# Kernel tuning notes

Hardware: AMD Instinct MI355X
Metric: run time of the kernel (lower is better)

The kernel has to match this reference:

```python
import jax, jax.numpy as jnp
import numpy as np

D = 1024   # hidden_size
H = 16     # n_head
K = 64     # head_size
B = 4
T = 1024
LAYER_ID = 12
NUM_LAYERS = 24
D_MIX = 32
D_DECAY = 64


def setup_inputs() -> dict:
    key = jax.random.key(0)
    ks = jax.random.split(key, 12)
    r01 = LAYER_ID / (NUM_LAYERS - 1)          # ratio_0_to_1
    r10 = 1.0 - LAYER_ID / NUM_LAYERS          # ratio_1_to_almost0
    ddd = jnp.arange(D, dtype=jnp.float32) / D
    maa = lambda p: (1.0 - ddd ** p).reshape(1, 1, D)
    inp = {}
    inp['x'] = jax.random.normal(ks[0], (B, T, D), jnp.float32)
    inp['time_maa_x'] = maa(r10)
    inp['time_maa_w'] = maa(r10)
    inp['time_maa_k'] = maa(r10)
    inp['time_maa_v'] = (1.0 - (ddd ** r10 + 0.3 * r01)).reshape(1, 1, D)
    inp['time_maa_r'] = maa(0.5 * r10)
    inp['time_maa_g'] = maa(0.5 * r10)
    # torch inits time_maa_w1 to zeros (trivial); use small uniform like w2 for a non-degenerate test
    inp['time_maa_w1'] = jax.random.uniform(ks[1], (D, D_MIX * 5), jnp.float32, -0.01, 0.01)
    inp['time_maa_w2'] = jax.random.uniform(ks[2], (5, D_MIX, D), jnp.float32, -0.01, 0.01)
    n = jnp.arange(D, dtype=jnp.float32)
    inp['time_decay'] = (-6.0 + 5.0 * (n / (D - 1)) ** (0.7 + 1.3 * r01)).reshape(1, 1, D)
    inp['time_decay_w1'] = jax.random.uniform(ks[3], (D, D_DECAY), jnp.float32, -0.01, 0.01)
    inp['time_decay_w2'] = jax.random.uniform(ks[4], (D_DECAY, D), jnp.float32, -0.01, 0.01)
    for nm, kk in zip(['W_r', 'W_k', 'W_v', 'W_g', 'W_o'], ks[5:10]):
        inp[nm] = jax.random.normal(kk, (D, D), jnp.float32) * 0.02
    inp['ln_w'] = jnp.ones((D,), jnp.float32)
    inp['ln_b'] = jnp.zeros((D,), jnp.float32)
    return inp


def _bidir_shift(x):
    # (x[i-1] + x[i+1]) / 2 with zero padding at the boundaries
    left = jnp.pad(x[:, :-1, :], ((0, 0), (1, 0), (0, 0)))
    right = jnp.pad(x[:, 1:, :], ((0, 0), (0, 1), (0, 0)))
    return 0.5 * (left + right)


def _lion_attention(r, k, v, w):
    # r,k,v,w: (B,H,T,Khd), w = -exp(decay) <= 0
    Tn = r.shape[2]
    cs = jnp.cumsum(w, axis=2)
    cs_b = cs - w
    shift_f = cs[:, :, Tn // 2:Tn // 2 + 1, :]
    shift_b = cs_b[:, :, Tn // 2:Tn // 2 + 1, :]
    cf = jnp.clip(cs - shift_f, -60.0, 60.0)
    cb = jnp.clip(cs_b - shift_b, -60.0, 60.0)
    # A_fwd = tril(Q*e^{cf} @ (K*e^{-cf})^T); A_bwd = triu(Q*e^{-cb} @ (K*e^{cb})^T, 1)
    A_f = jnp.einsum('bhik,bhjk->bhij', r * jnp.exp(cf), k * jnp.exp(-cf))
    A_b = jnp.einsum('bhik,bhjk->bhij', r * jnp.exp(-cb), k * jnp.exp(cb))
    idx = jnp.arange(Tn)
    lower = idx[:, None] >= idx[None, :]   # tril incl. diagonal
    A = jnp.where(lower, A_f, A_b)         # == tril(A_f) + triu(A_b, 1)
    return jnp.einsum('bhij,bhjk->bhik', A, v)


def reference(x, time_maa_x, time_maa_w, time_maa_k, time_maa_v, time_maa_r, time_maa_g,
              time_maa_w1, time_maa_w2, time_decay, time_decay_w1, time_decay_w2,
              W_r, W_k, W_v, W_g, W_o, ln_w, ln_b):
    Bn, Tn, Dn = x.shape
    Hh, Kk = H, Dn // H
    dxprev = _bidir_shift(x) - x
    # data-dependent token-shift mixing coefficients (LoRA-style)
    xxx = jnp.tanh((x + dxprev * time_maa_x) @ time_maa_w1)          # (B,T,5*32)
    mm = jnp.einsum('btfm,fmd->fbtd', xxx.reshape(Bn, Tn, 5, D_MIX), time_maa_w2)
    mw, mk, mv, mr, mg = mm[0], mm[1], mm[2], mm[3], mm[4]
    xw = x + dxprev * (time_maa_w + mw)
    xk = x + dxprev * (time_maa_k + mk)
    xv = x + dxprev * (time_maa_v + mv)
    xr = x + dxprev * (time_maa_r + mr)
    xg = x + dxprev * (time_maa_g + mg)
    r = xr @ W_r.T
    k = xk @ W_k.T
    v = xv @ W_v.T
    g = jax.nn.silu(xg @ W_g.T)
    w = time_decay + jnp.tanh(xw @ time_decay_w1) @ time_decay_w2   # (B,T,D)
    to_h = lambda t: t.reshape(Bn, Tn, Hh, Kk).transpose(0, 2, 1, 3)
    y = _lion_attention(to_h(r), to_h(k), to_h(v), -jnp.exp(to_h(w)))
    y = y.transpose(0, 2, 1, 3).reshape(Bn * Tn, Dn)
    # GroupNorm(n_head groups, eps = 1e-5 * head_size_divisor^2)
    eps = 1e-5 * 64.0
    yg = y.reshape(Bn * Tn, Hh, Kk)
    mu = jnp.mean(yg, axis=-1, keepdims=True)
    var = jnp.var(yg, axis=-1, keepdims=True)
    yn = ((yg - mu) * jax.lax.rsqrt(var + eps)).reshape(Bn * Tn, Dn) * ln_w + ln_b
    y = yn.reshape(Bn, Tn, Dn)
    return (y * g) @ W_o.T
```

## Files before the change

### kernel.cpp

```cpp
#include <hip/hip_runtime.h>
#include <math.h>

#define NB 4
#define TT 1024
#define DD 1024
#define NTOK 4096
#define ND (NTOK*DD)

typedef __attribute__((ext_vector_type(8))) short bh8;
typedef __attribute__((ext_vector_type(4))) float fx4;

__device__ __forceinline__ unsigned short f2bf(float f) {
    unsigned int b = __float_as_uint(f);
    b += 0x7fffu + ((b >> 16) & 1u);
    return (unsigned short)(b >> 16);
}

__device__ __forceinline__ unsigned pkbf(float a, float b) {
#if __has_builtin(__builtin_amdgcn_cvt_pk_bf16_f32)
    auto r = __builtin_amdgcn_cvt_pk_bf16_f32(a, b);
    unsigned u;
    __builtin_memcpy(&u, &r, 4);
    return u;
#else
    return ((unsigned)f2bf(b) << 16) | f2bf(a);
#endif
}

#define GLD16(gp, lp) __builtin_amdgcn_global_load_lds( \
    (__attribute__((address_space(1))) void*)(gp), \
    (__attribute__((address_space(3))) void*)(lp), 16, 0, 0)

__global__ __launch_bounds__(256) void k_prep(const float* __restrict__ W_r, const float* __restrict__ W_k,
                                              const float* __restrict__ W_v, const float* __restrict__ W_g,
                                              const float* __restrict__ W_o,
                                              const float* __restrict__ w1, const float* __restrict__ dw1,
                                              const float* __restrict__ w2,
                                              unsigned short* __restrict__ Wrb, unsigned short* __restrict__ Wkb,
                                              unsigned short* __restrict__ Wvb, unsigned short* __restrict__ Wgb,
                                              unsigned short* __restrict__ Wob,
                                              unsigned short* __restrict__ w1T, unsigned short* __restrict__ dw1T,
                                              unsigned short* __restrict__ w2T16) {
    int y = blockIdx.y, bx = blockIdx.x, tid = threadIdx.x;
    if (y < 5) {
        if (bx >= 512) return;
        const float* s = (y == 0) ? W_r : (y == 1) ? W_k : (y == 2) ? W_v : (y == 3) ? W_g : W_o;
        unsigned short* d = (y == 0) ? Wrb : (y == 1) ? Wkb : (y == 2) ? Wvb : (y == 3) ? Wgb : Wob;
        int i = (bx * 256 + tid) * 8;
        float4 a = *(const float4*)(s + i);
        float4 b = *(const float4*)(s + i + 4);
        uint4 o;
        o.x = pkbf(a.x, a.y);
        o.y = pkbf(a.z, a.w);
        o.z = pkbf(b.x, b.y);
        o.w = pkbf(b.z, b.w);
        *(uint4*)(d + i) = o;
    } else if (y == 5) {
        int o = bx * 256 + tid;
        int r = o & 1023, c = o >> 10;
        w1T[o] = f2bf(w1[r * 160 + c]);
    } else {
        if (bx < 256) {
            int o = bx * 256 + tid;
            int r = o & 1023, c = o >> 10;
            dw1T[o] = f2bf(dw1[r * 64 + c]);
        } else if (bx < 276) {
            int wi = bx - 256;
            int f = wi >> 2;
            int d = (wi & 3) * 256 + tid;
#pragma unroll 8
            for (int m = 0; m < 32; m++)
                w2T16[(size_t)(f * 1024 + d) * 32 + m] = f2bf(w2[(size_t)(f * 32 + m) * 1024 + d]);
        }
    }
}

__global__ __launch_bounds__(256) void k_mixx(const float* __restrict__ x,
                                              const float* __restrict__ maa_x,
                                              unsigned short* __restrict__ xmix16) {
    int base = (blockIdx.x * 256 + threadIdx.x) * 4;
    int t = (base >> 10) & 1023;
    int d = base & 1023;
    float4 xv = *(const float4*)(x + base);
    float4 xm = (t > 0)    ? *(const float4*)(x + base - 1024) : make_float4(0, 0, 0, 0);
    float4 xp = (t < 1023) ? *(const float4*)(x + base + 1024) : make_float4(0, 0, 0, 0);
    float4 ma = *(const float4*)(maa_x + d);
    uint2 o;
    float a0 = xv.x + (0.5f * (xm.x + xp.x) - xv.x) * ma.x;
    float a1 = xv.y + (0.5f * (xm.y + xp.y) - xv.y) * ma.y;
    float a2 = xv.z + (0.5f * (xm.z + xp.z) - xv.z) * ma.z;
    float a3 = xv.w + (0.5f * (xm.w + xp.w) - xv.w) * ma.w;
    o.x = pkbf(a0, a1);
    o.y = pkbf(a2, a3);
    *(uint2*)(xmix16 + base) = o;
}

__global__ __launch_bounds__(64) void k_xxx2(const unsigned short* __restrict__ xmix16,
                                             const unsigned short* __restrict__ w1T,
                                             unsigned short* __restrict__ xxx16) {
    int lane = threadIdx.x;
    int l15 = lane & 15, qd = lane >> 4;
    int m0 = blockIdx.x * 16;
    fx4 acc[10];
#pragma unroll
    for (int nt = 0; nt < 10; nt++)
#pragma unroll
        for (int r = 0; r < 4; r++) acc[nt][r] = 0.f;
#pragma unroll 2
    for (int kb = 0; kb < 1024; kb += 32) {
        bh8 af = *(const bh8*)(xmix16 + (size_t)(m0 + l15) * 1024 + kb + qd * 8);
#pragma unroll
        for (int nt = 0; nt < 10; nt++) {
            bh8 bf = *(const bh8*)(w1T + (size_t)(nt * 16 + l15) * 1024 + kb + qd * 8);
            acc[nt] = __builtin_amdgcn_mfma_f32_16x16x32_bf16(af, bf, acc[nt], 0, 0, 0);
        }
    }
#pragma unroll
    for (int nt = 0; nt < 10; nt++)
#pragma unroll
        for (int r = 0; r < 4; r++)
            xxx16[(size_t)(m0 + qd * 4 + r) * 160 + nt * 16 + l15] = f2bf(tanhf(acc[nt][r]));
}

__global__ __launch_bounds__(256, 2) void k_mmix(const float* __restrict__ x,
                                                 const unsigned short* __restrict__ xxx16,
                                                 const unsigned short* __restrict__ w2T16,
                                                 const float* __restrict__ maa_w,
                                                 const float* __restrict__ maa_k,
                                                 const float* __restrict__ maa_v,
                                                 const float* __restrict__ maa_r,
                                                 const float* __restrict__ maa_g,
                                                 unsigned short* __restrict__ xw16,
                                                 unsigned short* __restrict__ xk16,
                                                 unsigned short* __restrict__ xv16,
                                                 unsigned short* __restrict__ xr16,
                                                 unsigned short* __restrict__ xg16) {
    int tid = threadIdx.x;
    int w = tid >> 6, lane = tid & 63, l15 = lane & 15, qd = lane >> 4;
    int n0 = blockIdx.x * 64;
    int m0w = blockIdx.y * 128 + w * 32;
    const float* maap[5] = {maa_w, maa_k, maa_v, maa_r, maa_g};
    unsigned short* outp[5] = {xw16, xk16, xv16, xr16, xg16};
    float xin[8][4], dxv[8][4];
#pragma unroll
    for (int mi = 0; mi < 2; mi++)
#pragma unroll
        for (int r = 0; r < 4; r++) {
            int tok = m0w + mi * 16 + qd * 4 + r;
            int t = tok & 1023;
#pragma unroll
            for (int ni = 0; ni < 4; ni++) {
                int d = n0 + ni * 16 + l15;
                size_t idx = (size_t)tok * 1024 + d;
                float xv = x[idx];
                float xm1 = (t > 0)    ? x[idx - 1024] : 0.f;
                float xp1 = (t < 1023) ? x[idx + 1024] : 0.f;
                xin[mi * 4 + r][ni] = xv;
                dxv[mi * 4 + r][ni] = 0.5f * (xm1 + xp1) - xv;
            }
        }
#pragma unroll
    for (int f = 0; f < 5; f++) {
        bh8 af[2], bf[4];
#pragma unroll
        for (int mi = 0; mi < 2; mi++)
            af[mi] = *(const bh8*)(xxx16 + (size_t)(m0w + mi * 16 + l15) * 160 + f * 32 + qd * 8);
#pragma unroll
        for (int ni = 0; ni < 4; ni++)
            bf[ni] = *(const bh8*)(w2T16 + (size_t)(f * 1024 + n0 + ni * 16 + l15) * 32 + qd * 8);
        fx4 acc[2][4];
#pragma unroll
        for (int mi = 0; mi < 2; mi++)
#pragma unroll
            for (int ni = 0; ni < 4; ni++) {
#pragma unroll
                for (int r = 0; r < 4; r++) acc[mi][ni][r] = 0.f;
                acc[mi][ni] = __builtin_amdgcn_mfma_f32_16x16x32_bf16(af[mi], bf[ni], acc[mi][ni], 0, 0, 0);
            }
        const float* maa = maap[f];
        unsigned short* op = outp[f];
#pragma unroll
        for (int ni = 0; ni < 4; ni++) {
            float mv = maa[n0 + ni * 16 + l15];
#pragma unroll
            for (int mi = 0; mi < 2; mi++)
#pragma unroll
                for (int r = 0; r < 4; r++) {
                    float o = xin[mi * 4 + r][ni] + dxv[mi * 4 + r][ni] * (mv + acc[mi][ni][r]);
                    op[(size_t)(m0w + mi * 16 + qd * 4 + r) * 1024 + n0 + ni * 16 + l15] = f2bf(o);
                }
        }
    }
}

__global__ __launch_bounds__(64) void k_dec1m(const unsigned short* __restrict__ xw16,
                                              const unsigned short* __restrict__ dw1T,
                                              float* __restrict__ dech) {
    int lane = threadIdx.x;
    int l15 = lane & 15, qd = lane >> 4;
    int m0 = blockIdx.x * 16;
    fx4 acc[4];
#pragma unroll
    for (int nt = 0; nt < 4; nt++)
#pragma unroll
        for (int r = 0; r < 4; r++) acc[nt][r] = 0.f;
#pragma unroll 2
    for (int kb = 0; kb < 1024; kb += 32) {
        bh8 af = *(const bh8*)(xw16 + (size_t)(m0 + l15) * 1024 + kb + qd * 8);
#pragma unroll
        for (int nt = 0; nt < 4; nt++) {
            bh8 bf = *(const bh8*)(dw1T + (size_t)(nt * 16 + l15) * 1024 + kb + qd * 8);
            acc[nt] = __builtin_amdgcn_mfma_f32_16x16x32_bf16(af, bf, acc[nt], 0, 0, 0);
        }
    }
#pragma unroll
    for (int nt = 0; nt < 4; nt++)
#pragma unroll
        for (int r = 0; r < 4; r++)
            dech[(size_t)(m0 + qd * 4 + r) * 64 + nt * 16 + l15] = tanhf(acc[nt][r]);
}

__global__ __launch_bounds__(256) void k_dec2(const float* __restrict__ dech,
                                              const float* __restrict__ dw2,
                                              const float* __restrict__ tdec,
                                              float* __restrict__ ew) {
    __shared__ float hl[8][64];
    int tid = threadIdx.x;
    int tok0 = blockIdx.x * 8;
    {
        int l = tid;        hl[l >> 6][l & 63] = dech[tok0 * 64 + l];
        l = tid + 256;      hl[l >> 6][l & 63] = dech[tok0 * 64 + l];
    }
    __syncthreads();
#pragma unroll 1
    for (int c = 0; c < 4; c++) {
        int d = c * 256 + tid;
        float acc[8] = {};
#pragma unroll 8
        for (int j = 0; j < 64; j++) {
            float wv = dw2[j * 1024 + d];
#pragma unroll
            for (int g = 0; g < 8; g++) acc[g] = fmaf(hl[g][j], wv, acc[g]);
        }
        float td = tdec[d];
#pragma unroll
        for (int g = 0; g < 8; g++) ew[(tok0 + g) * 1024 + d] = -expf(td + acc[g]);
    }
}

__global__ __launch_bounds__(64) void k_scan1(const float* __restrict__ ew, float* __restrict__ segsum) {
    int bx = blockIdx.x;
    int b = bx >> 9, seg = (bx >> 4) & 31, dch = bx & 15;
    int d = dch * 64 + threadIdx.x;
    size_t base = ((size_t)(b * 1024 + seg * 32)) * 1024 + d;
    float s = 0.f;
#pragma unroll 8
    for (int t = 0; t < 32; t++) s += ew[base + (size_t)t * 1024];
    segsum[(b * 32 + seg) * 1024 + d] = s;
}

__global__ __launch_bounds__(64) void k_scan3(const float* __restrict__ ew, const float* __restrict__ segsum,
                                              float* __restrict__ cf, float* __restrict__ cb) {
    int bx = blockIdx.x;
    int b = bx >> 9, seg = (bx >> 4) & 31, dch = bx & 15;
    int d = dch * 64 + threadIdx.x;
    float run = 0.f, pre = 0.f, off16 = 0.f;
#pragma unroll
    for (int s = 0; s < 32; s++) {
        float tv = segsum[(b * 32 + s) * 1024 + d];
        if (s == seg) pre = run;
        if (s == 16) off16 = run;
        run += tv;
    }
    float e512 = ew[((size_t)(b * 1024 + 512)) * 1024 + d];
    float sb = off16;
    float sf = off16 + e512;
    float cum = pre;
    size_t base = ((size_t)(b * 1024 + seg * 32)) * 1024 + d;
#pragma unroll 4
    for (int t = 0; t < 32; t++) {
        float prev = cum;
        cum += ew[base + (size_t)t * 1024];
        cf[base + (size_t)t * 1024] = fminf(fmaxf(cum - sf, -60.f), 60.f);
        cb[base + (size_t)t * 1024] = fminf(fmaxf(prev - sb, -60.f), 60.f);
    }
}

__device__ __forceinline__ void gemm_body(const unsigned short* __restrict__ A,
                                          const unsigned short* __restrict__ W,
                                          int m0, int n0, int mode,
                                          float* __restrict__ Cf,
                                          unsigned short* __restrict__ O1,
                                          unsigned short* __restrict__ O2,
                                          const float* __restrict__ cfp,
                                          const float* __restrict__ cbp,
                                          char* smem) {
    int tid = threadIdx.x;
    int w = tid >> 6, lane = tid & 63, l15 = lane & 15, qd = lane >> 4;
    int wm = w >> 1, wn = w & 1;
    fx4 acc[4][4];
#pragma unroll
    for (int mt = 0; mt < 4; mt++)
#pragma unroll
        for (int nt = 0; nt < 4; nt++)
#pragma unroll
            for (int r = 0; r < 4; r++) acc[mt][nt][r] = 0.f;
    unsigned short* sA = (unsigned short*)smem;
    unsigned short* sB = (unsigned short*)(smem + 8192);
    int rowA = tid >> 2, cA = tid & 3;
    for (int kb = 0; kb < 1024; kb += 32) {
        __syncthreads();
        GLD16(A + (size_t)(m0 + rowA) * 1024 + kb + cA * 8,      sA + w * 512);
        GLD16(A + (size_t)(m0 + 64 + rowA) * 1024 + kb + cA * 8, sA + 2048 + w * 512);
        GLD16(W + (size_t)(n0 + rowA) * 1024 + kb + cA * 8,      sB + w * 512);
        GLD16(W + (size_t)(n0 + 64 + rowA) * 1024 + kb + cA * 8, sB + 2048 + w * 512);
        __syncthreads();
        bh8 af[4], bfr[4];
#pragma unroll
        for (int mt = 0; mt < 4; mt++)
            af[mt] = *(const bh8*)(sA + (wm * 64 + mt * 16 + l15) * 32 + qd * 8);
#pragma unroll
        for (int nt = 0; nt < 4; nt++)
            bfr[nt] = *(const bh8*)(sB + (wn * 64 + nt * 16 + l15) * 32 + qd * 8);
#pragma unroll
        for (int mt = 0; mt < 4; mt++)
#pragma unroll
            for (int nt = 0; nt < 4; nt++)
                acc[mt][nt] = __builtin_amdgcn_mfma_f32_16x16x32_bf16(af[mt], bfr[nt], acc[mt][nt], 0, 0, 0);
    }
    int mb = m0 + wm * 64, nb = n0 + wn * 64;
    if (mode <= 1) {
#pragma unroll
        for (int mt = 0; mt < 4; mt++)
#pragma unroll
            for (int nt = 0; nt < 4; nt++) {
                fx4 s = acc[mt][nt];
#pragma unroll
                for (int r = 0; r < 4; r++) {
                    float v = s[r];
                    if (mode == 1) v = v / (1.f + __expf(-v));
                    Cf[(size_t)(mb + mt * 16 + qd * 4 + r) * 1024 + nb + nt * 16 + l15] = v;
                }
            }
    } else if (mode <= 3) {
        float s1 = (mode == 2) ? 1.f : -1.f;
#pragma unroll
        for (int mt = 0; mt < 4; mt++)
#pragma unroll
            for (int nt = 0; nt < 4; nt++) {
                fx4 s = acc[mt][nt];
#pragma unroll
                for (int r = 0; r < 4; r++) {
                    size_t idx = (size_t)(mb + mt * 16 + qd * 4 + r) * 1024 + nb + nt * 16 + l15;
                    float v = s[r];
                    O1[idx] = f2bf(v * __expf(s1 * cfp[idx]));
                    O2[idx] = f2bf(v * __expf(-s1 * cbp[idx]));
                }
            }
    } else {
        __syncthreads();
        unsigned short* T = (unsigned short*)smem;
#pragma unroll
        for (int mt = 0; mt < 4; mt++)
#pragma unroll
            for (int nt = 0; nt < 4; nt++) {
                fx4 s = acc[mt][nt];
                int dl = wn * 64 + nt * 16 + l15;
                int tl = wm * 64 + mt * 16 + qd * 4;
                uint2 pk;
                pk.x = pkbf(s[0], s[1]);
                pk.y = pkbf(s[2], s[3]);
                *(uint2*)(T + dl * 136 + tl) = pk;
            }
        __syncthreads();
        int dl = tid >> 1, hf = tid & 1;
        int bq = m0 >> 10, t0 = m0 & 1023;
#pragma unroll
        for (int i = 0; i < 8; i++) {
            uint4 vv4 = *(const uint4*)(T + dl * 136 + hf * 64 + i * 8);
            *(uint4*)(O1 + (size_t)(bq * 1024 + n0 + dl) * 1024 + t0 + hf * 64 + i * 8) = vv4;
        }
    }
}

__global__ __launch_bounds__(256, 2) void k_gemm4(const unsigned short* __restrict__ xr16,
                                                  const unsigned short* __restrict__ xk16,
                                                  const unsigned short* __restrict__ xv16,
                                                  const unsigned short* __restrict__ xg16,
                                                  const unsigned short* __restrict__ Wrb,
                                                  const unsigned short* __restrict__ Wkb,
                                                  const unsigned short* __restrict__ Wvb,
                                                  const unsigned short* __restrict__ Wgb,
                                                  unsigned short* __restrict__ qf, unsigned short* __restrict__ qb,
                                                  unsigned short* __restrict__ kf, unsigned short* __restrict__ kb,
                                                  unsigned short* __restrict__ vvt,
                                                  float* __restrict__ gg,
                                                  const float* __restrict__ cf, const float* __restrict__ cb) {
    __shared__ __align__(16) char smem[34816];
    int m0 = (blockIdx.x >> 3) * 128, n0 = (blockIdx.x & 7) * 128;
    int y = blockIdx.y;
    if (y == 0)      gemm_body(xr16, Wrb, m0, n0, 2, nullptr, qf, qb, cf, cb, smem);
    else if (y == 1) gemm_body(xk16, Wkb, m0, n0, 3, nullptr, kf, kb, cf, cb, smem);
    else if (y == 2) gemm_body(xv16, Wvb, m0, n0, 4, nullptr, vvt, nullptr, nullptr, nullptr, smem);
    else             gemm_body(xg16, Wgb, m0, n0, 1, gg, nullptr, nullptr, nullptr, nullptr, smem);
}

__global__ __launch_bounds__(256, 2) void k_gemmo(const unsigned short* __restrict__ z16,
                                                  const unsigned short* __restrict__ Wob,
                                                  float* __restrict__ out) {
    __shared__ __align__(16) char smem[34816];
    gemm_body(z16, Wob, (blockIdx.x >> 3) * 128, (blockIdx.x & 7) * 128, 0, out,
              nullptr, nullptr, nullptr, nullptr, smem);
}

__global__ __launch_bounds__(256, 2) void k_attn(const unsigned short* __restrict__ qf,
                                                 const unsigned short* __restrict__ qb,
                                                 const unsigned short* __restrict__ kf,
                                                 const unsigned short* __restrict__ kb,
                                                 const unsigned short* __restrict__ vvt,
                                                 float* __restrict__ y) {
    __shared__ __align__(16) char smem[16384];
    unsigned short* sK = (unsigned short*)smem;
    unsigned short* sV = (unsigned short*)(smem + 8192);
    int tid = threadIdx.x;
    int w = tid >> 6, lane = tid & 63, l15 = lane & 15, qd = lane >> 4;
    int bid = blockIdx.x;
    int bh = (bid & 7) + ((bid >> 6) << 3);
    int ib = (bid >> 3) & 7;
    int b = bh >> 4, h = bh & 15;
    int i0w = ib * 128 + w * 32;
    int bt0 = b * 1024;
    const unsigned short* vrow = vvt + (size_t)(b * 1024 + h * 64 + w * 16 + l15) * 1024 + qd * 8;
    int fmax = (i0w + 31) >> 6;
    int bmin = i0w >> 6;
    int srcA = l15 + ((lane & 16) << 1);
    int srcB = srcA + 16;
    fx4 yacc[4][2];
#pragma unroll
    for (int mt = 0; mt < 4; mt++)
#pragma unroll
        for (int nt = 0; nt < 2; nt++)
#pragma unroll
            for (int r = 0; r < 4; r++) yacc[mt][nt][r] = 0.f;

    for (int phase = 0; phase < 2; phase++) {
        const unsigned short* Q = phase ? qb : qf;
        const unsigned short* K = phase ? kb : kf;
        bh8 qfr[2][2];
#pragma unroll
        for (int nt = 0; nt < 2; nt++)
#pragma unroll
            for (int ks = 0; ks < 2; ks++)
                qfr[nt][ks] = *(const bh8*)(Q + (size_t)(bt0 + i0w + nt * 16 + l15) * 1024
                                              + h * 64 + ks * 32 + qd * 8);
        int jlo = phase == 0 ? 0 : 2 * ib;
        int jhi = phase == 0 ? 2 * ib + 1 : 15;
        const unsigned short* krow = K + (size_t)(bt0 + w * 16 + l15) * 1024 + h * 64 + qd * 8;
        for (int jt = jlo; jt <= jhi; jt++) {
            int jb = jt * 64;
            __syncthreads();
            GLD16(krow + (size_t)jb * 1024,        sK + w * 512);
            GLD16(krow + (size_t)jb * 1024 + 32,   sK + 2048 + w * 512);
            GLD16(vrow + jb,                        sV + w * 512);
            GLD16(vrow + jb + 32,                   sV + 2048 + w * 512);
            __syncthreads();
            bool active = (phase == 0) ? (jt <= fmax) : (jt >= bmin);
            if (!active) continue;
            bool needmask = (phase == 0) ? (jb + 63 > i0w) : (i0w + 31 >= jb);
            bh8 kc[8];
#pragma unroll
            for (int fi = 0; fi < 8; fi++)
                kc[fi] = *(const bh8*)(sK + fi * 512 + lane * 8);
            fx4 sacc[4][2];
#pragma unroll
            for (int mt = 0; mt < 4; mt++)
#pragma unroll
                for (int nt = 0; nt < 2; nt++)
#pragma unroll
                    for (int r = 0; r < 4; r++) sacc[mt][nt][r] = 0.f;
#pragma unroll
            for (int ks = 0; ks < 2; ks++)
#pragma unroll
                for (int mt = 0; mt < 4; mt++)
#pragma unroll
                    for (int nt = 0; nt < 2; nt++)
                        sacc[mt][nt] = __builtin_amdgcn_mfma_f32_16x16x32_bf16(kc[ks * 4 + mt], qfr[nt][ks], sacc[mt][nt], 0, 0, 0);
            uint2 pk[4][2];
#pragma unroll
            for (int mt = 0; mt < 4; mt++)
#pragma unroll
                for (int nt = 0; nt < 2; nt++) {
                    fx4 s = sacc[mt][nt];
                    if (needmask) {
                        int ii = i0w + nt * 16 + l15;
                        int jj0 = jb + mt * 16 + qd * 4;
#pragma unroll
                        for (int r = 0; r < 4; r++) {
                            bool keep = (phase == 0) ? (ii >= jj0 + r) : (ii < jj0 + r);
                            if (!keep) s[r] = 0.f;
                        }
                    }
                    pk[mt][nt].x = pkbf(s[0], s[1]);
                    pk[mt][nt].y = pkbf(s[2], s[3]);
                }
            bh8 vc[8];
#pragma unroll
            for (int fi = 0; fi < 8; fi++)
                vc[fi] = *(const bh8*)(sV + fi * 512 + lane * 8);
#pragma unroll
            for (int ks2 = 0; ks2 < 2; ks2++) {
#pragma unroll
                for (int nt = 0; nt < 2; nt++) {
                    int lox  = __shfl((int)pk[2 * ks2][nt].x,     srcA);
                    int hix  = __shfl((int)pk[2 * ks2 + 1][nt].x, srcA);
                    int loy  = __shfl((int)pk[2 * ks2][nt].y,     srcA);
                    int hiy  = __shfl((int)pk[2 * ks2 + 1][nt].y, srcA);
                    int lox2 = __shfl((int)pk[2 * ks2][nt].x,     srcB);
                    int hix2 = __shfl((int)pk[2 * ks2 + 1][nt].x, srcB);
                    int loy2 = __shfl((int)pk[2 * ks2][nt].y,     srcB);
                    int hiy2 = __shfl((int)pk[2 * ks2 + 1][nt].y, srcB);
                    union { int4 i; bh8 h; } cv;
                    cv.i.x = (qd & 2) ? hix  : lox;
                    cv.i.y = (qd & 2) ? hiy  : loy;
                    cv.i.z = (qd & 2) ? hix2 : lox2;
                    cv.i.w = (qd & 2) ? hiy2 : loy2;
#pragma unroll
                    for (int mt = 0; mt < 4; mt++)
                        yacc[mt][nt] = __builtin_amdgcn_mfma_f32_16x16x32_bf16(vc[ks2 * 4 + mt], cv.h, yacc[mt][nt], 0, 0, 0);
                }
            }
        }
    }
#pragma unroll
    for (int mt = 0; mt < 4; mt++)
#pragma unroll
        for (int nt = 0; nt < 2; nt++) {
            fx4 s = yacc[mt][nt];
            float4 o; o.x = s[0]; o.y = s[1]; o.z = s[2]; o.w = s[3];
            *(float4*)&y[(size_t)(bt0 + i0w + nt * 16 + l15) * 1024 + h * 64 + mt * 16 + qd * 4] = o;
        }
}

__global__ __launch_bounds__(256) void k_gn(const float* __restrict__ y,
                                            const float* __restrict__ g,
                                            const float* __restrict__ lnw,
                                            const float* __restrict__ lnb,
                                            unsigned short* __restrict__ z16) {
    int tid = threadIdx.x;
    int lane = tid & 63;
    int wv = tid >> 6;
    int group = blockIdx.x * 4 + wv;
    int tok = group >> 4, h = group & 15;
    int d = h * 64 + lane;
    size_t idx = (size_t)tok * 1024 + d;
    float val = y[idx];
    float s = val, s2 = val * val;
#pragma unroll
    for (int off = 32; off > 0; off >>= 1) {
        s  += __shfl_xor(s, off, 64);
        s2 += __shfl_xor(s2, off, 64);
    }
    float mu = s * (1.f / 64.f);
    float var = s2 * (1.f / 64.f) - mu * mu;
    float inv = rsqrtf(var + 6.4e-4f);
    float yn = (val - mu) * inv * lnw[d] + lnb[d];
    z16[idx] = f2bf(yn * g[idx]);
}

extern "C" void kernel_launch(void* const* d_in, const int* in_sizes, int n_in,
                              void* d_out, int out_size, void* d_ws, size_t ws_size,
                              hipStream_t stream) {
    const float* x     = (const float*)d_in[0];
    const float* maa_x = (const float*)d_in[1];
    const float* maa_w = (const float*)d_in[2];
    const float* maa_k = (const float*)d_in[3];
    const float* maa_v = (const float*)d_in[4];
    const float* maa_r = (const float*)d_in[5];
    const float* maa_g = (const float*)d_in[6];
    const float* w1    = (const float*)d_in[7];
    const float* w2    = (const float*)d_in[8];
    const float* tdec  = (const float*)d_in[9];
    const float* dw1   = (const float*)d_in[10];
    const float* dw2   = (const float*)d_in[11];
    const float* W_r   = (const float*)d_in[12];
    const float* W_k   = (const float*)d_in[13];
    const float* W_v   = (const float*)d_in[14];
    const float* W_g   = (const float*)d_in[15];
    const float* W_o   = (const float*)d_in[16];
    const float* lnw   = (const float*)d_in[17];
    const float* lnb   = (const float*)d_in[18];

    float* ws = (float*)d_ws;
    size_t o = 0;
    float* dech   = ws + o; o += 262144;
    float* segsum = ws + o; o += 131072;
    float* ew     = ws + o; o += 4194304;
    float* cf     = ws + o; o += 4194304;
    float* cb     = ws + o; o += 4194304;
    float* gg     = ws + o; o += 4194304;
    unsigned short* us = (unsigned short*)(ws + o);
    size_t u = 0;
    unsigned short* xmix16 = us + u; u += 4194304;
    unsigned short* xw16 = us + u; u += 4194304;
    unsigned short* xr16 = us + u; u += 4194304;
    unsigned short* xk16 = us + u; u += 4194304;
    unsigned short* xv16 = us + u; u += 4194304;
    unsigned short* xg16 = us + u; u += 4194304;
    unsigned short* qf   = us + u; u += 4194304;
    unsigned short* qb   = us + u; u += 4194304;
    unsigned short* kf   = us + u; u += 4194304;
    unsigned short* kb   = us + u; u += 4194304;
    unsigned short* vvt  = us + u; u += 4194304;
    unsigned short* Wrb  = us + u; u += 1048576;
    unsigned short* Wkb  = us + u; u += 1048576;
    unsigned short* Wvb  = us + u; u += 1048576;
    unsigned short* Wgb  = us + u; u += 1048576;
    unsigned short* Wob  = us + u; u += 1048576;
    unsigned short* w1T  = us + u; u += 163840;
    unsigned short* dw1T = us + u; u += 65536;
    unsigned short* xxx16 = us + u; u += 655360;
    unsigned short* w2T16 = us + u; u += 163840;
    float* yb0 = cf;
    unsigned short* z16 = xr16;

    k_prep<<<dim3(640, 7), 256, 0, stream>>>(W_r, W_k, W_v, W_g, W_o, w1, dw1, w2,
                                             Wrb, Wkb, Wvb, Wgb, Wob, w1T, dw1T, w2T16);
    k_mixx<<<4096, 256, 0, stream>>>(x, maa_x, xmix16);
    k_xxx2<<<256, 64, 0, stream>>>(xmix16, w1T, xxx16);
    k_mmix<<<dim3(16, 32), 256, 0, stream>>>(x, xxx16, w2T16, maa_w, maa_k, maa_v, maa_r, maa_g,
                                             xw16, xk16, xv16, xr16, xg16);
    k_dec1m<<<256, 64, 0, stream>>>(xw16, dw1T, dech);
    k_dec2<<<512, 256, 0, stream>>>(dech, dw2, tdec, ew);
    k_scan1<<<2048, 64, 0, stream>>>(ew, segsum);
    k_scan3<<<2048, 64, 0, stream>>>(ew, segsum, cf, cb);
    k_gemm4<<<dim3(256, 4), 256, 0, stream>>>(xr16, xk16, xv16, xg16, Wrb, Wkb, Wvb, Wgb,
                                              qf, qb, kf, kb, vvt, gg, cf, cb);
    k_attn<<<512, 256, 0, stream>>>(qf, qb, kf, kb, vvt, yb0);
    k_gn<<<16384, 256, 0, stream>>>(yb0, gg, lnw, lnb, z16);
    k_gemmo<<<256, 256, 0, stream>>>(z16, Wob, (float*)d_out);
}
```

Baseline: 344.8 us.

## Rewrite projection GEMMs with 256x128 tiles, triple-buffered LDS and swizzle

Replaces the shared GEMM body with a version that uses 256x128 output tiles and a three-stage LDS ring. Global-to-LDS loads are issued two k-steps ahead, with vmcnt waits and a single barrier per step. LDS columns are XOR-swizzled to avoid bank conflicts, MFMA sections are wrapped in s_setprio, and block indices are remapped across XCDs. The larger tiles halve the grid, to 512 blocks for QKVG and 128 for the output GEMM, and use 72KB of LDS and more accumulator registers, which may cut occupancy and underfill the GPU on the output GEMM.

```diff
diff --git a/kernel.cpp b/kernel.cpp
--- a/kernel.cpp
+++ b/kernel.cpp
@@ -30,6 +30,8 @@
 #define GLD16(gp, lp) __builtin_amdgcn_global_load_lds( \
     (__attribute__((address_space(1))) void*)(gp), \
     (__attribute__((address_space(3))) void*)(lp), 16, 0, 0)
+
+#define BARF() do { __builtin_amdgcn_s_barrier(); asm volatile("" ::: "memory"); } while (0)
 
 __global__ __launch_bounds__(256) void k_prep(const float* __restrict__ W_r, const float* __restrict__ W_k,
                                               const float* __restrict__ W_v, const float* __restrict__ W_g,
@@ -286,131 +288,164 @@
     }
 }
 
-__device__ __forceinline__ void gemm_body(const unsigned short* __restrict__ A,
-                                          const unsigned short* __restrict__ W,
-                                          int m0, int n0, int mode,
-                                          float* __restrict__ Cf,
-                                          unsigned short* __restrict__ O1,
-                                          unsigned short* __restrict__ O2,
-                                          const float* __restrict__ cfp,
-                                          const float* __restrict__ cbp,
-                                          char* smem) {
+#define QST(slotoff, kbv) do { \
+    unsigned short* _sa = (unsigned short*)(smem + (slotoff)); \
+    unsigned short* _sb = _sa + 8192; \
+    GLD16(aSrc + (size_t)(kbv),             _sa + (w * 64) * 32); \
+    GLD16(aSrc + (size_t)(kbv) + 16 * 1024, _sa + (w * 64 + 16) * 32); \
+    GLD16(aSrc + (size_t)(kbv) + 32 * 1024, _sa + (w * 64 + 32) * 32); \
+    GLD16(aSrc + (size_t)(kbv) + 48 * 1024, _sa + (w * 64 + 48) * 32); \
+    GLD16(bSrc + (size_t)(kbv),             _sb + (w * 32) * 32); \
+    GLD16(bSrc + (size_t)(kbv) + 16 * 1024, _sb + (w * 32 + 16) * 32); \
+} while (0)
+
+__device__ __forceinline__ void gemm_v4(const unsigned short* __restrict__ A,
+                                        const unsigned short* __restrict__ W,
+                                        int m0, int n0, int mode,
+                                        float* __restrict__ Cf,
+                                        unsigned short* __restrict__ O1,
+                                        unsigned short* __restrict__ O2,
+                                        const float* __restrict__ cfp,
+                                        const float* __restrict__ cbp,
+                                        char* smem) {
     int tid = threadIdx.x;
-    int w = tid >> 6, lane = tid & 63, l15 = lane & 15, qd = lane >> 4;
+    int lane = tid & 63, w = tid >> 6;
+    int l15 = lane & 15, qd = lane >> 4;
     int wm = w >> 1, wn = w & 1;
-    fx4 acc[4][4];
-#pragma unroll
-    for (int mt = 0; mt < 4; mt++)
+    int lr = lane >> 2, lb = lane & 3;
+    int gblk = lb ^ ((lr >> 1) & 3);
+    const unsigned short* aSrc = A + (size_t)(m0 + w * 64 + lr) * 1024 + gblk * 8;
+    const unsigned short* bSrc = W + (size_t)(n0 + w * 32 + lr) * 1024 + gblk * 8;
+    int rc = (qd ^ ((l15 >> 1) & 3)) * 8;
+    int arow = (wm * 128 + l15) * 32 + rc;
+    int brow = (wn * 64 + l15) * 32 + rc;
+
+    fx4 acc[8][4];
+#pragma unroll
+    for (int mt = 0; mt < 8; mt++)
 #pragma unroll
         for (int nt = 0; nt < 4; nt++)
 #pragma unroll
             for (int r = 0; r < 4; r++) acc[mt][nt][r] = 0.f;
-    unsigned short* sA = (unsigned short*)smem;
-    unsigned short* sB = (unsigned short*)(smem + 8192);
-    int rowA = tid >> 2, cA = tid & 3;
-    for (int kb = 0; kb < 1024; kb += 32) {
-        __syncthreads();
-        GLD16(A + (size_t)(m0 + rowA) * 1024 + kb + cA * 8,      sA + w * 512);
-        GLD16(A + (size_t)(m0 + 64 + rowA) * 1024 + kb + cA * 8, sA + 2048 + w * 512);
-        GLD16(W + (size_t)(n0 + rowA) * 1024 + kb + cA * 8,      sB + w * 512);
-        GLD16(W + (size_t)(n0 + 64 + rowA) * 1024 + kb + cA * 8, sB + 2048 + w * 512);
-        __syncthreads();
-        bh8 af[4], bfr[4];
-#pragma unroll
-        for (int mt = 0; mt < 4; mt++)
-            af[mt] = *(const bh8*)(sA + (wm * 64 + mt * 16 + l15) * 32 + qd * 8);
-#pragma unroll
-        for (int nt = 0; nt < 4; nt++)
-            bfr[nt] = *(const bh8*)(sB + (wn * 64 + nt * 16 + l15) * 32 + qd * 8);
-#pragma unroll
-        for (int mt = 0; mt < 4; mt++)
+
+    QST(0, 0);
+    QST(24576, 32);
+    asm volatile("s_waitcnt vmcnt(6)" ::: "memory");
+    BARF();
+
+    int oc = 0, on = 24576, o2 = 49152;
+#pragma unroll 1
+    for (int t = 0; t < 32; ++t) {
+        if (t < 30) QST(o2, (t + 2) * 32);
+        const unsigned short* cA = (const unsigned short*)(smem + oc);
+        const unsigned short* cB = cA + 8192;
+        bh8 a[8], b[4];
+#pragma unroll
+        for (int mt = 0; mt < 8; ++mt) a[mt] = *(const bh8*)(cA + arow + mt * 512);
+#pragma unroll
+        for (int nt = 0; nt < 4; ++nt) b[nt] = *(const bh8*)(cB + brow + nt * 512);
+        __builtin_amdgcn_s_setprio(1);
+#pragma unroll
+        for (int nt = 0; nt < 4; ++nt)
+#pragma unroll
+            for (int mt = 0; mt < 8; ++mt)
+                acc[mt][nt] = __builtin_amdgcn_mfma_f32_16x16x32_bf16(a[mt], b[nt], acc[mt][nt], 0, 0, 0);
+        __builtin_amdgcn_s_setprio(0);
+        asm volatile("s_waitcnt lgkmcnt(0)" ::: "memory");
+        if (t < 30)       asm volatile("s_waitcnt vmcnt(6)" ::: "memory");
+        else if (t == 30) asm volatile("s_waitcnt vmcnt(0)" ::: "memory");
+        BARF();
+        int tmp = oc; oc = on; on = o2; o2 = tmp;
+    }
+
+    int mbase = m0 + wm * 128;
+    int nb = n0 + wn * 64;
+    if (mode <= 1) {
+#pragma unroll
+        for (int mt = 0; mt < 8; mt++)
 #pragma unroll
             for (int nt = 0; nt < 4; nt++)
-                acc[mt][nt] = __builtin_amdgcn_mfma_f32_16x16x32_bf16(af[mt], bfr[nt], acc[mt][nt], 0, 0, 0);
-    }
-    int mb = m0 + wm * 64, nb = n0 + wn * 64;
-    if (mode <= 1) {
-#pragma unroll
-        for (int mt = 0; mt < 4; mt++)
-#pragma unroll
-            for (int nt = 0; nt < 4; nt++) {
-                fx4 s = acc[mt][nt];
 #pragma unroll
                 for (int r = 0; r < 4; r++) {
-                    float v = s[r];
+                    float v = acc[mt][nt][r];
                     if (mode == 1) v = v / (1.f + __expf(-v));
-                    Cf[(size_t)(mb + mt * 16 + qd * 4 + r) * 1024 + nb + nt * 16 + l15] = v;
+                    Cf[(size_t)(mbase + mt * 16 + qd * 4 + r) * 1024 + nb + nt * 16 + l15] = v;
                 }
-            }
     } else if (mode <= 3) {
         float s1 = (mode == 2) ? 1.f : -1.f;
 #pragma unroll
-        for (int mt = 0; mt < 4; mt++)
-#pragma unroll
-            for (int nt = 0; nt < 4; nt++) {
-                fx4 s = acc[mt][nt];
+        for (int mt = 0; mt < 8; mt++)
+#pragma unroll
+            for (int nt = 0; nt < 4; nt++)
 #pragma unroll
                 for (int r = 0; r < 4; r++) {
-                    size_t idx = (size_t)(mb + mt * 16 + qd * 4 + r) * 1024 + nb + nt * 16 + l15;
-                    float v = s[r];
+                    size_t idx = (size_t)(mbase + mt * 16 + qd * 4 + r) * 1024 + nb + nt * 16 + l15;
+                    float v = acc[mt][nt][r];
                     O1[idx] = f2bf(v * __expf(s1 * cfp[idx]));
                     O2[idx] = f2bf(v * __expf(-s1 * cbp[idx]));
                 }
+    } else {
+        unsigned short* T = (unsigned short*)smem;
+        int bq = m0 >> 10, t0 = m0 & 1023;
+#pragma unroll
+        for (int mt = 0; mt < 8; mt++)
+#pragma unroll
+            for (int nt = 0; nt < 4; nt++) {
+                int dl = wn * 64 + nt * 16 + l15;
+                int tl = wm * 128 + mt * 16 + qd * 4;
+                uint2 pk2;
+                pk2.x = pkbf(acc[mt][nt][0], acc[mt][nt][1]);
+                pk2.y = pkbf(acc[mt][nt][2], acc[mt][nt][3]);
+                *(uint2*)(T + dl * 268 + tl) = pk2;
             }
-    } else {
-        __syncthreads();
-        unsigned short* T = (unsigned short*)smem;
-#pragma unroll
-        for (int mt = 0; mt < 4; mt++)
-#pragma unroll
-            for (int nt = 0; nt < 4; nt++) {
-                fx4 s = acc[mt][nt];
-                int dl = wn * 64 + nt * 16 + l15;
-                int tl = wm * 64 + mt * 16 + qd * 4;
-                uint2 pk;
-                pk.x = pkbf(s[0], s[1]);
-                pk.y = pkbf(s[2], s[3]);
-                *(uint2*)(T + dl * 136 + tl) = pk;
-            }
-        __syncthreads();
-        int dl = tid >> 1, hf = tid & 1;
-        int bq = m0 >> 10, t0 = m0 & 1023;
-#pragma unroll
-        for (int i = 0; i < 8; i++) {
-            uint4 vv4 = *(const uint4*)(T + dl * 136 + hf * 64 + i * 8);
-            *(uint4*)(O1 + (size_t)(bq * 1024 + n0 + dl) * 1024 + t0 + hf * 64 + i * 8) = vv4;
-        }
-    }
-}
-
-__global__ __launch_bounds__(256, 2) void k_gemm4(const unsigned short* __restrict__ xr16,
-                                                  const unsigned short* __restrict__ xk16,
-                                                  const unsigned short* __restrict__ xv16,
-                                                  const unsigned short* __restrict__ xg16,
-                                                  const unsigned short* __restrict__ Wrb,
-                                                  const unsigned short* __restrict__ Wkb,
-                                                  const unsigned short* __restrict__ Wvb,
-                                                  const unsigned short* __restrict__ Wgb,
-                                                  unsigned short* __restrict__ qf, unsigned short* __restrict__ qb,
-                                                  unsigned short* __restrict__ kf, unsigned short* __restrict__ kb,
-                                                  unsigned short* __restrict__ vvt,
-                                                  float* __restrict__ gg,
-                                                  const float* __restrict__ cf, const float* __restrict__ cb) {
-    __shared__ __align__(16) char smem[34816];
-    int m0 = (blockIdx.x >> 3) * 128, n0 = (blockIdx.x & 7) * 128;
-    int y = blockIdx.y;
-    if (y == 0)      gemm_body(xr16, Wrb, m0, n0, 2, nullptr, qf, qb, cf, cb, smem);
-    else if (y == 1) gemm_body(xk16, Wkb, m0, n0, 3, nullptr, kf, kb, cf, cb, smem);
-    else if (y == 2) gemm_body(xv16, Wvb, m0, n0, 4, nullptr, vvt, nullptr, nullptr, nullptr, smem);
-    else             gemm_body(xg16, Wgb, m0, n0, 1, gg, nullptr, nullptr, nullptr, nullptr, smem);
+        asm volatile("s_waitcnt lgkmcnt(0)" ::: "memory");
+        BARF();
+#pragma unroll
+        for (int i = 0; i < 16; ++i) {
+            int idx = i * 256 + tid;
+            int dd = idx >> 5, u = idx & 31;
+            uint4 vv = *(const uint4*)(T + dd * 268 + u * 8);
+            *(uint4*)(O1 + (size_t)(bq * 1024 + n0 + dd) * 1024 + t0 + u * 8) = vv;
+        }
+    }
+}
+
+__global__ __launch_bounds__(256, 2) void k_qkvg(const unsigned short* __restrict__ xr16,
+                                                 const unsigned short* __restrict__ xk16,
+                                                 const unsigned short* __restrict__ xv16,
+                                                 const unsigned short* __restrict__ xg16,
+                                                 const unsigned short* __restrict__ Wrb,
+                                                 const unsigned short* __restrict__ Wkb,
+                                                 const unsigned short* __restrict__ Wvb,
+                                                 const unsigned short* __restrict__ Wgb,
+                                                 unsigned short* __restrict__ qf, unsigned short* __restrict__ qb,
+                                                 unsigned short* __restrict__ kf, unsigned short* __restrict__ kb,
+                                                 unsigned short* __restrict__ vvt,
+                                                 float* __restrict__ gg,
+                                                 const float* __restrict__ cf, const float* __restrict__ cb) {
+    __shared__ __align__(16) char smem[73728];
+    int flat = blockIdx.x;
+    int wkid = (flat & 7) * 64 + (flat >> 3);
+    int gy = wkid >> 7;
+    int rem = wkid & 127;
+    int m0 = (rem >> 3) * 256, n0 = (rem & 7) * 128;
+    const unsigned short* Ap = (gy == 0) ? xr16 : (gy == 1) ? xk16 : (gy == 2) ? xv16 : xg16;
+    const unsigned short* Wp = (gy == 0) ? Wrb : (gy == 1) ? Wkb : (gy == 2) ? Wvb : Wgb;
+    int mode = (gy == 0) ? 2 : (gy == 1) ? 3 : (gy == 2) ? 4 : 1;
+    unsigned short* o1 = (gy == 0) ? qf : (gy == 1) ? kf : (gy == 2) ? vvt : nullptr;
+    unsigned short* o2 = (gy == 0) ? qb : (gy == 1) ? kb : nullptr;
+    float* cfo = (gy == 3) ? gg : nullptr;
+    gemm_v4(Ap, Wp, m0, n0, mode, cfo, o1, o2, cf, cb, smem);
 }
 
 __global__ __launch_bounds__(256, 2) void k_gemmo(const unsigned short* __restrict__ z16,
                                                   const unsigned short* __restrict__ Wob,
                                                   float* __restrict__ out) {
-    __shared__ __align__(16) char smem[34816];
-    gemm_body(z16, Wob, (blockIdx.x >> 3) * 128, (blockIdx.x & 7) * 128, 0, out,
-              nullptr, nullptr, nullptr, nullptr, smem);
+    __shared__ __align__(16) char smem[73728];
+    int flat = blockIdx.x;
+    int wkid = (flat & 7) * 16 + (flat >> 3);
+    int m0 = (wkid >> 3) * 256, n0 = (wkid & 7) * 128;
+    gemm_v4(z16, Wob, m0, n0, 0, out, nullptr, nullptr, nullptr, nullptr, smem);
 }
 
 __global__ __launch_bounds__(256, 2) void k_attn(const unsigned short* __restrict__ qf,
@@ -633,9 +668,9 @@
     k_dec2<<<512, 256, 0, stream>>>(dech, dw2, tdec, ew);
     k_scan1<<<2048, 64, 0, stream>>>(ew, segsum);
     k_scan3<<<2048, 64, 0, stream>>>(ew, segsum, cf, cb);
-    k_gemm4<<<dim3(256, 4), 256, 0, stream>>>(xr16, xk16, xv16, xg16, Wrb, Wkb, Wvb, Wgb,
-                                              qf, qb, kf, kb, vvt, gg, cf, cb);
+    k_qkvg<<<dim3(512), dim3(256), 0, stream>>>(xr16, xk16, xv16, xg16, Wrb, Wkb, Wvb, Wgb,
+                                                qf, qb, kf, kb, vvt, gg, cf, cb);
     k_attn<<<512, 256, 0, stream>>>(qf, qb, kf, kb, vvt, yb0);
     k_gn<<<16384, 256, 0, stream>>>(yb0, gg, lnw, lnb, z16);
-    k_gemmo<<<256, 256, 0, stream>>>(z16, Wob, (float*)d_out);
-}
+    k_gemmo<<<128, 256, 0, stream>>>(z16, Wob, (float*)d_out);
+}
```

Result: no change. 340.6 us (-1.2%).
